# Kernel optimization log

Hardware: AMD Instinct MI355X
Metric: run time of the kernel (lower is better)

Reference implementation:

```python
import jax, jax.numpy as jnp
import numpy as np

B, D, OUT, K = 2048, 256, 256, 16


def setup_inputs() -> dict:
    key = jax.random.key(0)
    k1, k2, k3, k4 = jax.random.split(key, 4)
    x = jax.random.normal(k1, (B, D), dtype=jnp.float32)
    values = jax.random.uniform(k2, (OUT, D, K), dtype=jnp.float32, minval=-0.05, maxval=0.05)
    skip_w = jax.random.normal(k3, (OUT, D), dtype=jnp.float32) * (1.0 / np.sqrt(D).astype(np.float32))
    skip_b = jax.random.normal(k4, (OUT,), dtype=jnp.float32) * 0.01
    return {"x": x, "values": values, "skip_w": skip_w, "skip_b": skip_b}


def reference(x, values, skip_w, skip_b):
    # x: (B, D); values: (OUT, D, K); skip_w: (OUT, D); skip_b: (OUT,)
    num_knots = values.shape[-1]
    grid = jnp.linspace(-1.0, 1.0, num_knots)  # (K,)
    xc = jnp.clip(x, -1.0, 1.0)
    # torch.bucketize(x, grid) with right=False == searchsorted side='left'
    right = jnp.searchsorted(grid, xc, side='left')
    left = jnp.clip(right - 1, 0, num_knots - 2)  # (B, D)
    right = left + 1
    g0 = grid[left]
    g1 = grid[right]
    w = (xc - g0) / (g1 - g0 + 1e-12)  # (B, D)
    # Gather spline values per (sample, input-dim) knot bucket.
    vt = jnp.transpose(values, (1, 2, 0))  # (D, K, OUT)
    dim_idx = jnp.arange(xc.shape[1])[None, :]  # (1, D)
    v_left = vt[dim_idx, left]    # (B, D, OUT)
    v_right = vt[dim_idx, right]  # (B, D, OUT)
    # Linear interpolation + sum over input dims.
    y = jnp.sum((1.0 - w)[..., None] * v_left + w[..., None] * v_right, axis=1)  # (B, OUT)
    # Skip connection on the clamped input (torch reassigns x = clamp(x) first).
    return y + xc @ skip_w.T + skip_b
```

## Files before the change

kernel.cpp:

```cpp
#include <hip/hip_runtime.h>
#include <hip/hip_bf16.h>


namespace {
constexpr int Bsz  = 2048;
constexpr int Din  = 256;
constexpr int Dout = 256;
constexpr int Kn   = 16;
constexpr int KKNOT = Din * Kn;
constexpr int Ksp   = KKNOT + Din;
constexpr int KB    = Ksp / 32;
constexpr int KBK   = KKNOT / 32;
constexpr float INV_H = 7.5f;
constexpr float Hgrid = 2.0f / 15.0f;

constexpr int NSPLIT = 17;
constexpr int SPS    = 8;
constexpr int MT     = Bsz / 64;
constexpr int TILE_F = 64 * 64;
constexpr int PELEM  = Bsz * Dout;
}

typedef __attribute__((ext_vector_type(8))) short shortx8;
typedef __attribute__((ext_vector_type(4))) float floatx4;

__device__ __forceinline__ unsigned int f2bf(float f) {
  __hip_bfloat16 h = __float2bfloat16(f);
  return (unsigned int)*reinterpret_cast<unsigned short*>(&h);
}
__device__ __forceinline__ float clamp1(float v) {
  return fminf(1.f, fmaxf(-1.f, v));
}
__device__ __forceinline__ unsigned int packbf(unsigned int e0, unsigned int e1) {
  return (e1 & 0xffff0000u) | (e0 >> 16);
}
__device__ __forceinline__ unsigned int rnd(float f) {
  return __float_as_uint(f) + 0x8000u;
}

__global__ __launch_bounds__(256) void kan_prep(
    const float* __restrict__ values, const float* __restrict__ skip_w,
    unsigned short* __restrict__ Wf) {
  const int tid = blockIdx.x * 256 + threadIdx.x;
  const int q  = tid & 3;
  const int n  = (tid >> 2) & 15;
  const int og = (tid >> 6) & 15;
  const int kb = tid >> 10;
  const int o  = og * 16 + n;
  const int k0 = kb * 32 + q * 8;
  const float* src = (kb < KBK)
      ? values + (size_t)o * KKNOT + k0
      : skip_w + (size_t)o * Din + (k0 - KKNOT);
  const float4 v0 = *(const float4*)src;
  const float4 v1 = *(const float4*)(src + 4);
  const size_t chunk = (size_t)kb * 1024 + og * 64 + q * 16 + n;
  *(uint4*)(Wf + chunk * 8) = make_uint4(
      f2bf(v0.x) | (f2bf(v0.y) << 16), f2bf(v0.z) | (f2bf(v0.w) << 16),
      f2bf(v1.x) | (f2bf(v1.y) << 16), f2bf(v1.z) | (f2bf(v1.w) << 16));
}

__global__ __launch_bounds__(256) void kan_gemm(
    const float* __restrict__ x, const unsigned short* __restrict__ Wf,
    float* __restrict__ part) {
  __shared__ float sx[16 * 64];
  __shared__ __align__(16) unsigned short aLds[2][64 * 32];

  const int tid  = threadIdx.x;
  const int wave = tid >> 6, lane = tid & 63;
  const int ks   = blockIdx.x % NSPLIT;
  const int mi   = blockIdx.x / NSPLIT;
  const int m0   = mi * 64;
  const int og0  = wave * 4;
  const int kb0  = (ks < 16) ? ks * SPS : KBK;

  const int lrow = lane & 15, lq = lane >> 4;

  const int brow_k = tid & 63, bseg_k = tid >> 6;
  const int brow_s = tid >> 2, bseg_s = tid & 3;

  const uint4* B = (const uint4*)Wf;

  floatx4 acc[4][4] = {};
  uint4 bb[2][4];

  if (ks < 16) {
    const int row = tid >> 2, dq = tid & 3;
    const float4 v = *(const float4*)(x + (size_t)(m0 + row) * Din + ks * 16 + 4 * dq);
    sx[(4 * dq + 0) * 64 + row] = v.x;
    sx[(4 * dq + 1) * 64 + row] = v.y;
    sx[(4 * dq + 2) * 64 + row] = v.z;
    sx[(4 * dq + 3) * 64 + row] = v.w;
    __syncthreads();
  }

  #pragma unroll
  for (int j = 0; j < 4; ++j)
    bb[0][j] = B[(size_t)kb0 * 1024 + (og0 + j) * 64 + lane];

  for (int s = 0; s < SPS; ++s) {
    const int cur = s & 1;
    if (s + 1 < SPS) {
      #pragma unroll
      for (int j = 0; j < 4; ++j)
        bb[cur ^ 1][j] = B[(size_t)(kb0 + s + 1) * 1024 + (og0 + j) * 64 + lane];
    }

    if (ks < 16) {
      const int dloc = 2 * s + (bseg_k >> 1);
      const float xv = sx[dloc * 64 + brow_k];
      const float t  = (clamp1(xv) + 1.f) * INV_H;
      const float h0 = (float)((bseg_k & 1) * 8);
      unsigned int e[8];
      #pragma unroll
      for (int h = 0; h < 8; ++h)
        e[h] = rnd(fmaxf(0.f, 1.f - fabsf(t - (h0 + (float)h))));
      *(uint4*)((char*)&aLds[cur][0] + brow_k * 64 + bseg_k * 16) =
          make_uint4(packbf(e[0], e[1]), packbf(e[2], e[3]),
                     packbf(e[4], e[5]), packbf(e[6], e[7]));
    } else {
      const float* xp = x + (size_t)(m0 + brow_s) * Din + (kb0 + s - KBK) * 32 + bseg_s * 8;
      const float4 v0 = *(const float4*)xp;
      const float4 v1 = *(const float4*)(xp + 4);
      unsigned int e[8];
      e[0] = rnd(clamp1(v0.x)); e[1] = rnd(clamp1(v0.y));
      e[2] = rnd(clamp1(v0.z)); e[3] = rnd(clamp1(v0.w));
      e[4] = rnd(clamp1(v1.x)); e[5] = rnd(clamp1(v1.y));
      e[6] = rnd(clamp1(v1.z)); e[7] = rnd(clamp1(v1.w));
      *(uint4*)((char*)&aLds[cur][0] + brow_s * 64 + bseg_s * 16) =
          make_uint4(packbf(e[0], e[1]), packbf(e[2], e[3]),
                     packbf(e[4], e[5]), packbf(e[6], e[7]));
    }
    __syncthreads();

    shortx8 af[4];
    #pragma unroll
    for (int i = 0; i < 4; ++i)
      af[i] = *(const shortx8*)((const char*)&aLds[cur][0] + (16 * i + lrow) * 64 + lq * 16);

    #pragma unroll
    for (int j = 0; j < 4; ++j) {
      union { uint4 u; shortx8 s; } bc;
      bc.u = bb[cur][j];
      #pragma unroll
      for (int i = 0; i < 4; ++i)
        acc[i][j] = __builtin_amdgcn_mfma_f32_16x16x32_bf16(af[i], bc.s, acc[i][j], 0, 0, 0);
    }
  }

  float* P = part + (size_t)ks * PELEM + (size_t)(mi * 4 + wave) * TILE_F;
  #pragma unroll
  for (int i = 0; i < 4; ++i)
    #pragma unroll
    for (int j = 0; j < 4; ++j)
      *(floatx4*)&P[((i * 4 + j) * 64 + lane) * 4] = acc[i][j];
}

__global__ __launch_bounds__(256) void kan_reduce(
    const float* __restrict__ part, const float* __restrict__ skip_b,
    float* __restrict__ out) {
  const int tid = blockIdx.x * 256 + threadIdx.x;
  float4 a = make_float4(0.f, 0.f, 0.f, 0.f);
  #pragma unroll
  for (int s = 0; s < NSPLIT; ++s) {
    const float4 p = *(const float4*)(part + (size_t)s * PELEM + (size_t)tid * 4);
    a.x += p.x; a.y += p.y; a.z += p.z; a.w += p.w;
  }
  const int f4   = tid & 1023, tile = tid >> 10;
  const int ij   = f4 >> 6,   lane = f4 & 63;
  const int i    = ij >> 2,   j    = ij & 3;
  const int mi   = tile >> 2, ni   = tile & 3;
  const int b0   = mi * 64 + 16 * i + (lane >> 4) * 4;
  const int o    = ni * 64 + 16 * j + (lane & 15);
  const float sb = skip_b[o];
  out[(size_t)(b0 + 0) * Dout + o] = a.x + sb;
  out[(size_t)(b0 + 1) * Dout + o] = a.y + sb;
  out[(size_t)(b0 + 2) * Dout + o] = a.z + sb;
  out[(size_t)(b0 + 3) * Dout + o] = a.w + sb;
}

__device__ __forceinline__ void knot_interp(float xraw, float& xv, float& w, int& l) {
  xv = fminf(1.0f, fmaxf(-1.0f, xraw));
  float t = (xv + 1.0f) * INV_H;
  l = (int)ceilf(t) - 1;
  l = l < 0 ? 0 : (l > Kn - 2 ? Kn - 2 : l);
  float g0 = -1.0f + Hgrid * (float)l;
  w = (xv - g0) * INV_H;
}

__global__ __launch_bounds__(256) void prep_transpose(
    const float* __restrict__ values, const float* __restrict__ skip_w,
    float* __restrict__ vt, float* __restrict__ swt) {
  int idx = blockIdx.x * blockDim.x + threadIdx.x;
  if (idx < Din * Kn * Dout) {
    int k = idx & (Kn - 1);
    int d = (idx >> 4) & (Din - 1);
    int o = idx >> 12;
    vt[(d * Kn + k) * Dout + o] = values[idx];
  }
  if (idx < Dout * Din) {
    int d = idx & (Din - 1);
    int o = idx >> 8;
    swt[d * Dout + o] = skip_w[idx];
  }
}

__global__ __launch_bounds__(256) void kan_main(
    const float* __restrict__ x, const float* __restrict__ vt,
    const float* __restrict__ swt, const float* __restrict__ skip_b,
    float* __restrict__ out) {
  __shared__ float s_w[4][Din];
  __shared__ float s_x[4][Din];
  __shared__ int   s_l[4][Din];
  const int tid = threadIdx.x;
  const int b0  = blockIdx.x * 4;
  for (int i = tid; i < 4 * Din; i += 256) {
    int bb = i >> 8;
    int d  = i & (Din - 1);
    float xv, w; int l;
    knot_interp(x[(b0 + bb) * Din + d], xv, w, l);
    s_w[bb][d] = w; s_x[bb][d] = xv; s_l[bb][d] = l;
  }
  __syncthreads();
  const int g = tid >> 6, lane = tid & 63;
  const int o = lane << 2, b = b0 + g;
  float4 acc = make_float4(0.f, 0.f, 0.f, 0.f);
  for (int d = 0; d < Din; ++d) {
    const float w = s_w[g][d], xv = s_x[g][d];
    const int l = s_l[g][d];
    const float* base = vt + (d * Kn + l) * Dout + o;
    const float4 vl = *(const float4*)(base);
    const float4 vr = *(const float4*)(base + Dout);
    const float4 sw = *(const float4*)(swt + d * Dout + o);
    acc.x = fmaf(xv, sw.x, fmaf(w, vr.x - vl.x, acc.x + vl.x));
    acc.y = fmaf(xv, sw.y, fmaf(w, vr.y - vl.y, acc.y + vl.y));
    acc.z = fmaf(xv, sw.z, fmaf(w, vr.z - vl.z, acc.z + vl.z));
    acc.w = fmaf(xv, sw.w, fmaf(w, vr.w - vl.w, acc.w + vl.w));
  }
  const float4 bias = *(const float4*)(skip_b + o);
  acc.x += bias.x; acc.y += bias.y; acc.z += bias.z; acc.w += bias.w;
  *(float4*)(out + (size_t)b * Dout + o) = acc;
}

extern "C" void kernel_launch(void* const* d_in, const int* in_sizes, int n_in,
                              void* d_out, int out_size, void* d_ws, size_t ws_size,
                              hipStream_t stream) {
  (void)in_sizes; (void)n_in; (void)out_size;
  const float* x      = (const float*)d_in[0];
  const float* values = (const float*)d_in[1];
  const float* skip_w = (const float*)d_in[2];
  const float* skip_b = (const float*)d_in[3];
  float* out = (float*)d_out;

  const size_t wf_bytes   = (size_t)Dout * Ksp * sizeof(unsigned short);
  const size_t part_bytes = (size_t)NSPLIT * PELEM * sizeof(float);
  const size_t need_gemm  = wf_bytes + part_bytes;
  const size_t need_fb    = (size_t)(Din * Kn * Dout + Din * Dout) * sizeof(float);

  if (ws_size >= need_gemm) {
    unsigned short* Wf = (unsigned short*)d_ws;
    float* part = (float*)((char*)d_ws + wf_bytes);
    kan_prep<<<(KB * 1024) / 256, 256, 0, stream>>>(values, skip_w, Wf);
    kan_gemm<<<MT * NSPLIT, 256, 0, stream>>>(x, Wf, part);
    kan_reduce<<<PELEM / 4 / 256, 256, 0, stream>>>(part, skip_b, out);
  } else if (ws_size >= need_fb) {
    float* vt  = (float*)d_ws;
    float* swt = vt + Din * Kn * Dout;
    prep_transpose<<<(Din * Kn * Dout + 255) / 256, 256, 0, stream>>>(values, skip_w, vt, swt);
    kan_main<<<Bsz / 4, 256, 0, stream>>>(x, vt, swt, skip_b, out);
  }
}
```

Before: 81.21 us.

## Retile KAN GEMM to 32x128 blocks with 4-way K split and pipelined A staging

The block tile shrinks from 64 rows by all 256 outputs to 32 rows by 128 outputs, and the K split drops from 17 to 4, so each block now runs 34 K-steps instead of 8. The A tile (hat-basis or clamped skip values) for the next step is built during the current step's MFMAs, with padded LDS rows (AROW=40) to reduce bank conflicts. The x-to-shared transpose stage is removed and x is read straight from global memory. The reduce kernel now sums 4 partial slabs instead of 17, which cuts partial-buffer traffic, but each wave does less MFMA work per B load and the B weight stream is reread by twice as many row tiles.

```diff
diff --git a/kernel.cpp b/kernel.cpp
--- a/kernel.cpp
+++ b/kernel.cpp
@@ -14,11 +14,10 @@
 constexpr float INV_H = 7.5f;
 constexpr float Hgrid = 2.0f / 15.0f;
 
-constexpr int NSPLIT = 17;
-constexpr int SPS    = 8;
-constexpr int MT     = Bsz / 64;
-constexpr int TILE_F = 64 * 64;
+constexpr int NSPLIT = 4;
+constexpr int SPS    = KB / NSPLIT;
 constexpr int PELEM  = Bsz * Dout;
+constexpr int AROW   = 40;
 }
 
 typedef __attribute__((ext_vector_type(8))) short shortx8;
@@ -62,97 +61,106 @@
 __global__ __launch_bounds__(256) void kan_gemm(
     const float* __restrict__ x, const unsigned short* __restrict__ Wf,
     float* __restrict__ part) {
-  __shared__ float sx[16 * 64];
-  __shared__ __align__(16) unsigned short aLds[2][64 * 32];
+  __shared__ __align__(16) unsigned short aLds[2][32 * AROW];
 
   const int tid  = threadIdx.x;
   const int wave = tid >> 6, lane = tid & 63;
-  const int ks   = blockIdx.x % NSPLIT;
-  const int mi   = blockIdx.x / NSPLIT;
-  const int m0   = mi * 64;
-  const int og0  = wave * 4;
-  const int kb0  = (ks < 16) ? ks * SPS : KBK;
+  const int bl   = blockIdx.x;
+  const int ks   = bl & 3;
+  const int nb   = (bl >> 2) & 1;
+  const int mi   = bl >> 3;
+  const int m0   = mi * 32;
+  const int og0  = nb * 8 + wave * 2;
+  const int kb0  = ks * SPS;
 
   const int lrow = lane & 15, lq = lane >> 4;
 
-  const int brow_k = tid & 63, bseg_k = tid >> 6;
-  const int brow_s = tid >> 2, bseg_s = tid & 3;
+  const int brow = tid >> 3;
+  const int bseg = tid & 7;
+  const float h0 = (float)((bseg & 3) * 4);
+  const int   bds = bseg >> 2;
+  const float* xrow = x + (size_t)(m0 + brow) * Din;
 
   const uint4* B = (const uint4*)Wf;
 
-  floatx4 acc[4][4] = {};
-  uint4 bb[2][4];
-
-  if (ks < 16) {
-    const int row = tid >> 2, dq = tid & 3;
-    const float4 v = *(const float4*)(x + (size_t)(m0 + row) * Din + ks * 16 + 4 * dq);
-    sx[(4 * dq + 0) * 64 + row] = v.x;
-    sx[(4 * dq + 1) * 64 + row] = v.y;
-    sx[(4 * dq + 2) * 64 + row] = v.z;
-    sx[(4 * dq + 3) * 64 + row] = v.w;
-    __syncthreads();
-  }
+  floatx4 acc[2][2] = {};
+  uint4 bb[2][2];
+  float4 px[2];
 
   #pragma unroll
-  for (int j = 0; j < 4; ++j)
+  for (int j = 0; j < 2; ++j)
     bb[0][j] = B[(size_t)kb0 * 1024 + (og0 + j) * 64 + lane];
+  if (kb0 < KBK) px[0].x = xrow[kb0 * 2 + bds];
+  else           px[0]   = *(const float4*)(xrow + (kb0 - KBK) * 32 + bseg * 4);
+
+  {
+    unsigned short* dst = &aLds[0][brow * AROW + bseg * 4];
+    if (kb0 < KBK) {
+      const float t = (clamp1(px[0].x) + 1.f) * INV_H;
+      unsigned int e0 = rnd(fmaxf(0.f, 1.f - fabsf(t - h0)));
+      unsigned int e1 = rnd(fmaxf(0.f, 1.f - fabsf(t - (h0 + 1.f))));
+      unsigned int e2 = rnd(fmaxf(0.f, 1.f - fabsf(t - (h0 + 2.f))));
+      unsigned int e3 = rnd(fmaxf(0.f, 1.f - fabsf(t - (h0 + 3.f))));
+      *(uint2*)dst = make_uint2(packbf(e0, e1), packbf(e2, e3));
+    } else {
+      *(uint2*)dst = make_uint2(
+          packbf(rnd(clamp1(px[0].x)), rnd(clamp1(px[0].y))),
+          packbf(rnd(clamp1(px[0].z)), rnd(clamp1(px[0].w))));
+    }
+  }
+  __syncthreads();
 
   for (int s = 0; s < SPS; ++s) {
-    const int cur = s & 1;
+    const int cur = s & 1, nxt = cur ^ 1;
+    const int kbn = kb0 + s + 1;
+
     if (s + 1 < SPS) {
       #pragma unroll
-      for (int j = 0; j < 4; ++j)
-        bb[cur ^ 1][j] = B[(size_t)(kb0 + s + 1) * 1024 + (og0 + j) * 64 + lane];
-    }
-
-    if (ks < 16) {
-      const int dloc = 2 * s + (bseg_k >> 1);
-      const float xv = sx[dloc * 64 + brow_k];
-      const float t  = (clamp1(xv) + 1.f) * INV_H;
-      const float h0 = (float)((bseg_k & 1) * 8);
-      unsigned int e[8];
-      #pragma unroll
-      for (int h = 0; h < 8; ++h)
-        e[h] = rnd(fmaxf(0.f, 1.f - fabsf(t - (h0 + (float)h))));
-      *(uint4*)((char*)&aLds[cur][0] + brow_k * 64 + bseg_k * 16) =
-          make_uint4(packbf(e[0], e[1]), packbf(e[2], e[3]),
-                     packbf(e[4], e[5]), packbf(e[6], e[7]));
-    } else {
-      const float* xp = x + (size_t)(m0 + brow_s) * Din + (kb0 + s - KBK) * 32 + bseg_s * 8;
-      const float4 v0 = *(const float4*)xp;
-      const float4 v1 = *(const float4*)(xp + 4);
-      unsigned int e[8];
-      e[0] = rnd(clamp1(v0.x)); e[1] = rnd(clamp1(v0.y));
-      e[2] = rnd(clamp1(v0.z)); e[3] = rnd(clamp1(v0.w));
-      e[4] = rnd(clamp1(v1.x)); e[5] = rnd(clamp1(v1.y));
-      e[6] = rnd(clamp1(v1.z)); e[7] = rnd(clamp1(v1.w));
-      *(uint4*)((char*)&aLds[cur][0] + brow_s * 64 + bseg_s * 16) =
-          make_uint4(packbf(e[0], e[1]), packbf(e[2], e[3]),
-                     packbf(e[4], e[5]), packbf(e[6], e[7]));
-    }
-    __syncthreads();
-
-    shortx8 af[4];
+      for (int j = 0; j < 2; ++j)
+        bb[nxt][j] = B[(size_t)kbn * 1024 + (og0 + j) * 64 + lane];
+      if (kbn < KBK) px[nxt].x = xrow[kbn * 2 + bds];
+      else           px[nxt]   = *(const float4*)(xrow + (kbn - KBK) * 32 + bseg * 4);
+    }
+
+    shortx8 af[2];
     #pragma unroll
-    for (int i = 0; i < 4; ++i)
-      af[i] = *(const shortx8*)((const char*)&aLds[cur][0] + (16 * i + lrow) * 64 + lq * 16);
-
+    for (int i = 0; i < 2; ++i)
+      af[i] = *(const shortx8*)((const char*)&aLds[cur][0] +
+                                (16 * i + lrow) * (AROW * 2) + lq * 16);
     #pragma unroll
-    for (int j = 0; j < 4; ++j) {
+    for (int j = 0; j < 2; ++j) {
       union { uint4 u; shortx8 s; } bc;
       bc.u = bb[cur][j];
       #pragma unroll
-      for (int i = 0; i < 4; ++i)
+      for (int i = 0; i < 2; ++i)
         acc[i][j] = __builtin_amdgcn_mfma_f32_16x16x32_bf16(af[i], bc.s, acc[i][j], 0, 0, 0);
     }
-  }
-
-  float* P = part + (size_t)ks * PELEM + (size_t)(mi * 4 + wave) * TILE_F;
+
+    if (s + 1 < SPS) {
+      unsigned short* dst = &aLds[nxt][brow * AROW + bseg * 4];
+      if (kbn < KBK) {
+        const float t = (clamp1(px[nxt].x) + 1.f) * INV_H;
+        unsigned int e0 = rnd(fmaxf(0.f, 1.f - fabsf(t - h0)));
+        unsigned int e1 = rnd(fmaxf(0.f, 1.f - fabsf(t - (h0 + 1.f))));
+        unsigned int e2 = rnd(fmaxf(0.f, 1.f - fabsf(t - (h0 + 2.f))));
+        unsigned int e3 = rnd(fmaxf(0.f, 1.f - fabsf(t - (h0 + 3.f))));
+        *(uint2*)dst = make_uint2(packbf(e0, e1), packbf(e2, e3));
+      } else {
+        *(uint2*)dst = make_uint2(
+            packbf(rnd(clamp1(px[nxt].x)), rnd(clamp1(px[nxt].y))),
+            packbf(rnd(clamp1(px[nxt].z)), rnd(clamp1(px[nxt].w))));
+      }
+      __syncthreads();
+    }
+  }
+
+  const int wtile = (mi * 2 + nb) * 4 + wave;
+  float* P = part + (size_t)ks * PELEM + (size_t)wtile * 1024;
   #pragma unroll
-  for (int i = 0; i < 4; ++i)
+  for (int i = 0; i < 2; ++i)
     #pragma unroll
-    for (int j = 0; j < 4; ++j)
-      *(floatx4*)&P[((i * 4 + j) * 64 + lane) * 4] = acc[i][j];
+    for (int j = 0; j < 2; ++j)
+      *(floatx4*)&P[((i * 2 + j) * 64 + lane) * 4] = acc[i][j];
 }
 
 __global__ __launch_bounds__(256) void kan_reduce(
@@ -165,13 +173,15 @@
     const float4 p = *(const float4*)(part + (size_t)s * PELEM + (size_t)tid * 4);
     a.x += p.x; a.y += p.y; a.z += p.z; a.w += p.w;
   }
-  const int f4   = tid & 1023, tile = tid >> 10;
-  const int ij   = f4 >> 6,   lane = f4 & 63;
-  const int i    = ij >> 2,   j    = ij & 3;
-  const int mi   = tile >> 2, ni   = tile & 3;
-  const int b0   = mi * 64 + 16 * i + (lane >> 4) * 4;
-  const int o    = ni * 64 + 16 * j + (lane & 15);
-  const float sb = skip_b[o];
+  const int f4    = tid & 255, wtile = tid >> 8;
+  const int ij    = f4 >> 6,  lane  = f4 & 63;
+  const int i     = ij >> 1,  j     = ij & 1;
+  const int mi    = wtile >> 3;
+  const int nb    = (wtile >> 2) & 1;
+  const int wave  = wtile & 3;
+  const int b0    = mi * 32 + 16 * i + (lane >> 4) * 4;
+  const int o     = nb * 128 + wave * 32 + 16 * j + (lane & 15);
+  const float sb  = skip_b[o];
   out[(size_t)(b0 + 0) * Dout + o] = a.x + sb;
   out[(size_t)(b0 + 1) * Dout + o] = a.y + sb;
   out[(size_t)(b0 + 2) * Dout + o] = a.z + sb;
@@ -260,7 +270,7 @@
     unsigned short* Wf = (unsigned short*)d_ws;
     float* part = (float*)((char*)d_ws + wf_bytes);
     kan_prep<<<(KB * 1024) / 256, 256, 0, stream>>>(values, skip_w, Wf);
-    kan_gemm<<<MT * NSPLIT, 256, 0, stream>>>(x, Wf, part);
+    kan_gemm<<<(Bsz / 32) * 2 * NSPLIT, 256, 0, stream>>>(x, Wf, part);
     kan_reduce<<<PELEM / 4 / 256, 256, 0, stream>>>(part, skip_b, out);
   } else if (ws_size >= need_fb) {
     float* vt  = (float*)d_ws;
```

After: 131.3 us. +61.6%, slower.
